# Performance work log

Hardware: AMD Instinct MI355X
Metric: run time of the kernel (lower is better)

The kernel has to match this reference:

```python
import jax, jax.numpy as jnp
import numpy as np

B, T, QD, AD = 64, 2048, 1024, 256


def setup_inputs() -> dict:
    key = jax.random.key(0)
    k1, k2, k3, k4, k5 = jax.random.split(key, 5)
    encoder_seq_proj = jax.random.normal(k1, (B, T, AD), dtype=jnp.float32)
    query = jax.random.normal(k2, (B, QD), dtype=jnp.float32)
    chars = jax.random.randint(k3, (B, T), 0, 60, dtype=jnp.int64)
    # learned params (nn.Linear, bias=False): weight shape (out, in)
    Wq = jax.random.normal(k4, (AD, QD), dtype=jnp.float32) / np.sqrt(QD)
    v = jax.random.normal(k5, (AD,), dtype=jnp.float32) / np.sqrt(AD)
    return {"encoder_seq_proj": encoder_seq_proj, "query": query,
            "chars": chars, "t": 1, "Wq": Wq, "v": v}


def reference(encoder_seq_proj, query, chars, t, Wq, v):
    # query: (B, QD) -> unsqueeze to (B, 1, QD) is implicit via broadcasting
    processed_query = jnp.einsum('bq,aq->ba', query, Wq)            # (B, AD)
    # broadcast add + tanh + v-reduction (large intermediate (B,T,AD))
    energies = jnp.einsum('bta,a->bt',
                          jnp.tanh(processed_query[:, None, :] + encoder_seq_proj),
                          v)                                          # (B, T)
    energies = energies * (chars != 0).astype(energies.dtype)
    alignment = jax.nn.softmax(energies, axis=1)                     # (B, T)
    return alignment
```

## Files before the change

kernel.cpp:

```cpp
#include <hip/hip_runtime.h>
#include <math.h>

#define BB 64
#define TT 2048
#define QD 1024
#define AD 256

__device__ __forceinline__ float tanh_fast(float x) {
    float e = __expf(2.0f * x);
    return 1.0f - __fdividef(2.0f, e + 1.0f);
}

__global__ __launch_bounds__(256) void pq_kernel(const float* __restrict__ query,
                                                 const float* __restrict__ Wq,
                                                 float* __restrict__ pq) {
    int w    = (blockIdx.x * blockDim.x + threadIdx.x) >> 6;
    int lane = threadIdx.x & 63;
    int b = w >> 8;
    int a = w & (AD - 1);
    const float4* qrow = (const float4*)(query + (size_t)b * QD);
    const float4* wrow = (const float4*)(Wq + (size_t)a * QD);
    float acc = 0.f;
    #pragma unroll
    for (int i = 0; i < QD / 4 / 64; ++i) {
        float4 q4 = qrow[lane + i * 64];
        float4 w4 = wrow[lane + i * 64];
        acc += q4.x * w4.x + q4.y * w4.y + q4.z * w4.z + q4.w * w4.w;
    }
    #pragma unroll
    for (int off = 32; off > 0; off >>= 1)
        acc += __shfl_down(acc, off, 64);
    if (lane == 0) pq[w] = acc;
}

__global__ __launch_bounds__(256) void energy_kernel(const float* __restrict__ esp,
                                                     const float* __restrict__ pq,
                                                     const float* __restrict__ v,
                                                     const int* __restrict__ chars,
                                                     float* __restrict__ energies) {
    int w    = (blockIdx.x * blockDim.x + threadIdx.x) >> 6;
    int lane = threadIdx.x & 63;
    int b = w >> 11;
    const float4* erow = (const float4*)(esp + (size_t)w * AD);
    const float4* prow = (const float4*)(pq + (size_t)b * AD);
    const float4* vrow = (const float4*)v;
    float4 e4 = erow[lane];
    float4 p4 = prow[lane];
    float4 v4 = vrow[lane];
    float s = tanh_fast(p4.x + e4.x) * v4.x
            + tanh_fast(p4.y + e4.y) * v4.y
            + tanh_fast(p4.z + e4.z) * v4.z
            + tanh_fast(p4.w + e4.w) * v4.w;
    #pragma unroll
    for (int off = 32; off > 0; off >>= 1)
        s += __shfl_down(s, off, 64);
    if (lane == 0) {
        energies[w] = (chars[w] != 0) ? s : 0.0f;
    }
}

__global__ __launch_bounds__(256) void softmax_kernel(float* __restrict__ io) {
    __shared__ float red[4];
    int tid  = threadIdx.x;
    int wave = tid >> 6, lane = tid & 63;
    float* row = io + (size_t)blockIdx.x * TT;
    float vals[8];
    float m = -INFINITY;
    #pragma unroll
    for (int i = 0; i < 8; ++i) {
        vals[i] = row[i * 256 + tid];
        m = fmaxf(m, vals[i]);
    }
    #pragma unroll
    for (int off = 32; off > 0; off >>= 1)
        m = fmaxf(m, __shfl_xor(m, off, 64));
    if (lane == 0) red[wave] = m;
    __syncthreads();
    m = fmaxf(fmaxf(red[0], red[1]), fmaxf(red[2], red[3]));
    __syncthreads();
    float s = 0.f;
    #pragma unroll
    for (int i = 0; i < 8; ++i) {
        vals[i] = __expf(vals[i] - m);
        s += vals[i];
    }
    #pragma unroll
    for (int off = 32; off > 0; off >>= 1)
        s += __shfl_xor(s, off, 64);
    if (lane == 0) red[wave] = s;
    __syncthreads();
    s = red[0] + red[1] + red[2] + red[3];
    float inv = __fdividef(1.0f, s);
    #pragma unroll
    for (int i = 0; i < 8; ++i)
        row[i * 256 + tid] = vals[i] * inv;
}

extern "C" void kernel_launch(void* const* d_in, const int* in_sizes, int n_in,
                              void* d_out, int out_size, void* d_ws, size_t ws_size,
                              hipStream_t stream) {
    const float* esp   = (const float*)d_in[0];
    const float* query = (const float*)d_in[1];
    const int*   chars = (const int*)d_in[2];
    const float* Wq    = (const float*)d_in[4];
    const float* v     = (const float*)d_in[5];
    float* out = (float*)d_out;
    float* pq  = (float*)d_ws;

    pq_kernel<<<(BB * AD) / 4, 256, 0, stream>>>(query, Wq, pq);
    energy_kernel<<<(BB * TT) / 4, 256, 0, stream>>>(esp, pq, v, chars, out);
    softmax_kernel<<<BB, 256, 0, stream>>>(out);
}
```

Before: 40.94 us.

## Register-tile projection GEMV, batch four rows per wave in energy, widen softmax

The query projection now computes a 4x4 tile of (batch, attention) outputs per wave, so each query and weight row loaded from memory is reused four times. The energy kernel has each wave process four time steps, loading pq and v once and using vectorized int4/float4 for the mask and output. The softmax runs 1024 threads per row with float2 loads. These changes cut redundant global loads and launch granularity, at the cost of higher register pressure and fewer blocks in flight.

```diff
diff --git a/kernel.cpp b/kernel.cpp
--- a/kernel.cpp
+++ b/kernel.cpp
@@ -14,23 +14,48 @@
 __global__ __launch_bounds__(256) void pq_kernel(const float* __restrict__ query,
                                                  const float* __restrict__ Wq,
                                                  float* __restrict__ pq) {
-    int w    = (blockIdx.x * blockDim.x + threadIdx.x) >> 6;
+    int wg   = (blockIdx.x * blockDim.x + threadIdx.x) >> 6;
     int lane = threadIdx.x & 63;
-    int b = w >> 8;
-    int a = w & (AD - 1);
-    const float4* qrow = (const float4*)(query + (size_t)b * QD);
-    const float4* wrow = (const float4*)(Wq + (size_t)a * QD);
-    float acc = 0.f;
+    int b0 = (wg >> 6) * 4;
+    int a0 = (wg & 63) * 4;
+    float4 qr[4][4];
     #pragma unroll
-    for (int i = 0; i < QD / 4 / 64; ++i) {
-        float4 q4 = qrow[lane + i * 64];
-        float4 w4 = wrow[lane + i * 64];
-        acc += q4.x * w4.x + q4.y * w4.y + q4.z * w4.z + q4.w * w4.w;
+    for (int i = 0; i < 4; ++i) {
+        const float4* qrow = (const float4*)(query + (size_t)(b0 + i) * QD);
+        #pragma unroll
+        for (int k = 0; k < 4; ++k) qr[i][k] = qrow[lane + k * 64];
+    }
+    float acc[4][4];
+    #pragma unroll
+    for (int j = 0; j < 4; ++j) {
+        const float4* wrow = (const float4*)(Wq + (size_t)(a0 + j) * QD);
+        float4 w4[4];
+        #pragma unroll
+        for (int k = 0; k < 4; ++k) w4[k] = wrow[lane + k * 64];
+        #pragma unroll
+        for (int i = 0; i < 4; ++i) {
+            float a = 0.f;
+            #pragma unroll
+            for (int k = 0; k < 4; ++k)
+                a += qr[i][k].x * w4[k].x + qr[i][k].y * w4[k].y
+                   + qr[i][k].z * w4[k].z + qr[i][k].w * w4[k].w;
+            acc[i][j] = a;
+        }
     }
     #pragma unroll
     for (int off = 32; off > 0; off >>= 1)
-        acc += __shfl_down(acc, off, 64);
-    if (lane == 0) pq[w] = acc;
+        #pragma unroll
+        for (int i = 0; i < 4; ++i)
+            #pragma unroll
+            for (int j = 0; j < 4; ++j)
+                acc[i][j] += __shfl_down(acc[i][j], off, 64);
+    if (lane == 0) {
+        #pragma unroll
+        for (int i = 0; i < 4; ++i) {
+            float4 r = make_float4(acc[i][0], acc[i][1], acc[i][2], acc[i][3]);
+            ((float4*)(pq + (size_t)(b0 + i) * AD))[a0 >> 2] = r;
+        }
+    }
 }
 
 __global__ __launch_bounds__(256) void energy_kernel(const float* __restrict__ esp,
@@ -38,62 +63,69 @@
                                                      const float* __restrict__ v,
                                                      const int* __restrict__ chars,
                                                      float* __restrict__ energies) {
-    int w    = (blockIdx.x * blockDim.x + threadIdx.x) >> 6;
+    int wg   = (blockIdx.x * blockDim.x + threadIdx.x) >> 6;
     int lane = threadIdx.x & 63;
-    int b = w >> 11;
-    const float4* erow = (const float4*)(esp + (size_t)w * AD);
-    const float4* prow = (const float4*)(pq + (size_t)b * AD);
-    const float4* vrow = (const float4*)v;
-    float4 e4 = erow[lane];
-    float4 p4 = prow[lane];
-    float4 v4 = vrow[lane];
-    float s = tanh_fast(p4.x + e4.x) * v4.x
-            + tanh_fast(p4.y + e4.y) * v4.y
-            + tanh_fast(p4.z + e4.z) * v4.z
-            + tanh_fast(p4.w + e4.w) * v4.w;
+    int w0 = wg * 4;
+    int b  = w0 >> 11;
+    const float4* erow = (const float4*)(esp + (size_t)w0 * AD);
+    float4 e4[4];
+    #pragma unroll
+    for (int j = 0; j < 4; ++j) e4[j] = erow[j * 64 + lane];
+    float4 p4 = ((const float4*)(pq + (size_t)b * AD))[lane];
+    float4 v4 = ((const float4*)v)[lane];
+    float s[4];
+    #pragma unroll
+    for (int j = 0; j < 4; ++j) {
+        s[j] = tanh_fast(p4.x + e4[j].x) * v4.x
+             + tanh_fast(p4.y + e4[j].y) * v4.y
+             + tanh_fast(p4.z + e4[j].z) * v4.z
+             + tanh_fast(p4.w + e4[j].w) * v4.w;
+    }
     #pragma unroll
     for (int off = 32; off > 0; off >>= 1)
-        s += __shfl_down(s, off, 64);
+        #pragma unroll
+        for (int j = 0; j < 4; ++j)
+            s[j] += __shfl_down(s[j], off, 64);
     if (lane == 0) {
-        energies[w] = (chars[w] != 0) ? s : 0.0f;
+        int4 cc = *(const int4*)(chars + w0);
+        float4 r;
+        r.x = cc.x ? s[0] : 0.f;
+        r.y = cc.y ? s[1] : 0.f;
+        r.z = cc.z ? s[2] : 0.f;
+        r.w = cc.w ? s[3] : 0.f;
+        *(float4*)(energies + w0) = r;
     }
 }
 
-__global__ __launch_bounds__(256) void softmax_kernel(float* __restrict__ io) {
-    __shared__ float red[4];
+__global__ __launch_bounds__(1024) void softmax_kernel(float* __restrict__ io) {
+    __shared__ float red[16];
     int tid  = threadIdx.x;
     int wave = tid >> 6, lane = tid & 63;
     float* row = io + (size_t)blockIdx.x * TT;
-    float vals[8];
-    float m = -INFINITY;
-    #pragma unroll
-    for (int i = 0; i < 8; ++i) {
-        vals[i] = row[i * 256 + tid];
-        m = fmaxf(m, vals[i]);
-    }
+    float2 vv = ((float2*)row)[tid];
+    float m = fmaxf(vv.x, vv.y);
     #pragma unroll
     for (int off = 32; off > 0; off >>= 1)
         m = fmaxf(m, __shfl_xor(m, off, 64));
     if (lane == 0) red[wave] = m;
     __syncthreads();
-    m = fmaxf(fmaxf(red[0], red[1]), fmaxf(red[2], red[3]));
+    float mm = red[0];
+    #pragma unroll
+    for (int i = 1; i < 16; ++i) mm = fmaxf(mm, red[i]);
     __syncthreads();
-    float s = 0.f;
-    #pragma unroll
-    for (int i = 0; i < 8; ++i) {
-        vals[i] = __expf(vals[i] - m);
-        s += vals[i];
-    }
+    float e0 = __expf(vv.x - mm);
+    float e1 = __expf(vv.y - mm);
+    float s = e0 + e1;
     #pragma unroll
     for (int off = 32; off > 0; off >>= 1)
         s += __shfl_xor(s, off, 64);
     if (lane == 0) red[wave] = s;
     __syncthreads();
-    s = red[0] + red[1] + red[2] + red[3];
-    float inv = __fdividef(1.0f, s);
+    float ss = 0.f;
     #pragma unroll
-    for (int i = 0; i < 8; ++i)
-        row[i * 256 + tid] = vals[i] * inv;
+    for (int i = 0; i < 16; ++i) ss += red[i];
+    float inv = __fdividef(1.0f, ss);
+    ((float2*)row)[tid] = make_float2(e0 * inv, e1 * inv);
 }
 
 extern "C" void kernel_launch(void* const* d_in, const int* in_sizes, int n_in,
@@ -107,7 +139,7 @@
     float* out = (float*)d_out;
     float* pq  = (float*)d_ws;
 
-    pq_kernel<<<(BB * AD) / 4, 256, 0, stream>>>(query, Wq, pq);
-    energy_kernel<<<(BB * TT) / 4, 256, 0, stream>>>(esp, pq, v, chars, out);
-    softmax_kernel<<<BB, 256, 0, stream>>>(out);
+    pq_kernel<<<256, 256, 0, stream>>>(query, Wq, pq);
+    energy_kernel<<<(BB * TT) / 16, 256, 0, stream>>>(esp, pq, v, chars, out);
+    softmax_kernel<<<BB, 1024, 0, stream>>>(out);
 }
```

Measured after the change: 34.85 us (median of 2 runs). 1.17x faster.
